# Kernel optimization log

Hardware: AMD Instinct MI355X
Metric: run time of the kernel (lower is better)

The kernel has to match this reference:

```python
import jax, jax.numpy as jnp
import numpy as np

B, TE, TD, H = 8, 512, 256, 256  # batch, enc len, dec len, hidden (He==Hd)

def setup_inputs() -> dict:
    key = jax.random.key(0)
    k1, k2, k3, k4, k5 = jax.random.split(key, 5)
    # Keras 'uniform' initializer: U(-0.05, 0.05)
    u = lambda k, s: jax.random.uniform(k, s, jnp.float32, -0.05, 0.05)
    return {
        "encoder_out_seq": jax.random.normal(k1, (B, TE, H), jnp.float32),
        "decoder_out_seq": jax.random.normal(k2, (B, TD, H), jnp.float32),
        "W_a": u(k3, (H, H)),
        "U_a": u(k4, (H, H)),
        "V_a": u(k5, (H, 1)),
    }

def reference(encoder_out_seq, decoder_out_seq, W_a, U_a, V_a):
    # Bahdanau additive attention, fully batched (same math as the per-step K.rnn loop)
    We = jnp.einsum('bih,hk->bik', encoder_out_seq, W_a)   # [B,Te,H]
    Uh = jnp.einsum('bjh,hk->bjk', decoder_out_seq, U_a)   # [B,Td,H]
    # energies: V_a^T tanh(We_i + Uh_j)  -> [B,Td,Te]
    t = jnp.tanh(We[:, None, :, :] + Uh[:, :, None, :])    # [B,Td,Te,H]
    e = jnp.einsum('bjih,h->bji', t, V_a[:, 0])             # [B,Td,Te]
    e = jax.nn.softmax(e, axis=-1)                          # softmax over encoder positions
    c = jnp.einsum('bji,bih->bjh', e, encoder_out_seq)      # [B,Td,H]
    return (c, e)
```

## Files before the change

kernel.cpp:

```cpp
#include <hip/hip_runtime.h>


#define BB 8
#define TE 512
#define TD 256
#define HH 256

#define EXP2F(x) __builtin_amdgcn_exp2f(x)
#define RCPF(x)  __builtin_amdgcn_rcpf(x)
#define KSCALE   2.8853900817779268f
#define NSC      (-2.8853900817779268f)

typedef __attribute__((ext_vector_type(8))) short short8_t;
typedef __attribute__((ext_vector_type(4))) float f32x4;

__device__ __forceinline__ unsigned short f2bf(float x) {
    unsigned int u = __float_as_uint(x);
    return (unsigned short)((u + 0x7FFFu + ((u >> 16) & 1u)) >> 16);
}
__device__ __forceinline__ float bf2f(unsigned short h) {
    return __uint_as_float(((unsigned int)h) << 16);
}

__global__ __launch_bounds__(256) void k_tw(
    const float* __restrict__ Wa, const float* __restrict__ Ua,
    unsigned short* __restrict__ Wth, unsigned short* __restrict__ Wtl)
{
    const int t    = threadIdx.x;
    const int s    = blockIdx.x >> 4;
    const int tile = blockIdx.x & 15;
    const int tk   = (tile >> 2) * 64;
    const int th   = (tile & 3) * 64;
    const float* W = s ? Ua : Wa;

    __shared__ float Ls[64][65];
    const int kr = t >> 4;
    const int hc = (t & 15) * 4;
    #pragma unroll
    for (int r = 0; r < 4; r++) {
        float4 v = *(const float4*)(W + (size_t)(tk + kr + 16 * r) * HH + th + hc);
        Ls[kr + 16 * r][hc + 0] = v.x; Ls[kr + 16 * r][hc + 1] = v.y;
        Ls[kr + 16 * r][hc + 2] = v.z; Ls[kr + 16 * r][hc + 3] = v.w;
    }
    __syncthreads();
    const int hr  = t >> 4;
    const int kc4 = (t & 15) * 4;
    #pragma unroll
    for (int r = 0; r < 4; r++) {
        const int hl = hr + 16 * r;
        float f0 = Ls[kc4 + 0][hl], f1 = Ls[kc4 + 1][hl];
        float f2 = Ls[kc4 + 2][hl], f3 = Ls[kc4 + 3][hl];
        ushort4 hi, lo;
        hi.x = f2bf(f0); lo.x = f2bf(f0 - bf2f(hi.x));
        hi.y = f2bf(f1); lo.y = f2bf(f1 - bf2f(hi.y));
        hi.z = f2bf(f2); lo.z = f2bf(f2 - bf2f(hi.z));
        hi.w = f2bf(f3); lo.w = f2bf(f3 - bf2f(hi.w));
        const size_t o = ((size_t)(s * 256 + th + hl)) * 256 + tk + kc4;
        *(ushort4*)(Wth + o) = hi;
        *(ushort4*)(Wtl + o) = lo;
    }
}

__global__ __launch_bounds__(256) void k_pre(
    const float* __restrict__ enc, const float* __restrict__ dec,
    const unsigned short* __restrict__ Wth, const unsigned short* __restrict__ Wtl,
    float* __restrict__ W4, float* __restrict__ Uhe)
{
    const int t  = threadIdx.x;
    const int it = blockIdx.x >> 2;
    const int ht = blockIdx.x & 3;
    const int i0 = it * 64;
    const int h0 = ht * 64;
    const bool is_enc = (i0 < BB * TE);
    const float* X = is_enc ? (enc + (size_t)i0 * HH)
                            : (dec + (size_t)(i0 - BB * TE) * HH);
    const int s = is_enc ? 0 : 1;
    const unsigned short* Ah = Wth + ((size_t)(s * 256 + h0)) * 256;
    const unsigned short* Al = Wtl + ((size_t)(s * 256 + h0)) * 256;

    __shared__ unsigned short At_h[64][40], At_l[64][40];
    __shared__ unsigned short Xs_h[64][40], Xs_l[64][40];

    const int sr = t >> 2;
    const int sq = (t & 3) * 8;

    const int wv = t >> 6, l = t & 63;
    const int wh = (wv & 1) * 32;
    const int wi = (wv >> 1) * 32;
    const int fr = l & 15;
    const int fk = (l >> 4) * 8;
    const int rq = l >> 4;

    f32x4 acc[2][2];
    #pragma unroll
    for (int a0 = 0; a0 < 2; a0++)
        #pragma unroll
        for (int a1 = 0; a1 < 2; a1++)
            acc[a0][a1] = (f32x4){0.f, 0.f, 0.f, 0.f};

    short8_t aH = *(const short8_t*)(Ah + (size_t)sr * 256 + sq);
    short8_t aL = *(const short8_t*)(Al + (size_t)sr * 256 + sq);
    float4   x0 = *(const float4*)(X + (size_t)sr * HH + sq);
    float4   x1 = *(const float4*)(X + (size_t)sr * HH + sq + 4);

    #pragma unroll
    for (int c = 0; c < 8; c++) {
        short8_t xh, xl;
        {
            unsigned short h;
            h = f2bf(x0.x); xh[0] = (short)h; xl[0] = (short)f2bf(x0.x - bf2f(h));
            h = f2bf(x0.y); xh[1] = (short)h; xl[1] = (short)f2bf(x0.y - bf2f(h));
            h = f2bf(x0.z); xh[2] = (short)h; xl[2] = (short)f2bf(x0.z - bf2f(h));
            h = f2bf(x0.w); xh[3] = (short)h; xl[3] = (short)f2bf(x0.w - bf2f(h));
            h = f2bf(x1.x); xh[4] = (short)h; xl[4] = (short)f2bf(x1.x - bf2f(h));
            h = f2bf(x1.y); xh[5] = (short)h; xl[5] = (short)f2bf(x1.y - bf2f(h));
            h = f2bf(x1.z); xh[6] = (short)h; xl[6] = (short)f2bf(x1.z - bf2f(h));
            h = f2bf(x1.w); xh[7] = (short)h; xl[7] = (short)f2bf(x1.w - bf2f(h));
        }
        __syncthreads();
        *(short8_t*)&At_h[sr][sq] = aH;
        *(short8_t*)&At_l[sr][sq] = aL;
        *(short8_t*)&Xs_h[sr][sq] = xh;
        *(short8_t*)&Xs_l[sr][sq] = xl;
        if (c < 7) {
            const int kc = (c + 1) * 32;
            aH = *(const short8_t*)(Ah + (size_t)sr * 256 + kc + sq);
            aL = *(const short8_t*)(Al + (size_t)sr * 256 + kc + sq);
            x0 = *(const float4*)(X + (size_t)sr * HH + kc + sq);
            x1 = *(const float4*)(X + (size_t)sr * HH + kc + sq + 4);
        }
        __syncthreads();
        #pragma unroll
        for (int fm = 0; fm < 2; fm++) {
            short8_t a_h = *(const short8_t*)&At_h[wh + 16 * fm + fr][fk];
            short8_t a_l = *(const short8_t*)&At_l[wh + 16 * fm + fr][fk];
            #pragma unroll
            for (int fn = 0; fn < 2; fn++) {
                short8_t b_h = *(const short8_t*)&Xs_h[wi + 16 * fn + fr][fk];
                short8_t b_l = *(const short8_t*)&Xs_l[wi + 16 * fn + fr][fk];
                acc[fm][fn] = __builtin_amdgcn_mfma_f32_16x16x32_bf16(a_h, b_h, acc[fm][fn], 0, 0, 0);
                acc[fm][fn] = __builtin_amdgcn_mfma_f32_16x16x32_bf16(a_h, b_l, acc[fm][fn], 0, 0, 0);
                acc[fm][fn] = __builtin_amdgcn_mfma_f32_16x16x32_bf16(a_l, b_h, acc[fm][fn], 0, 0, 0);
            }
        }
    }

    #pragma unroll
    for (int fm = 0; fm < 2; fm++) {
        #pragma unroll
        for (int fn = 0; fn < 2; fn++) {
            f32x4 v = acc[fm][fn];
            float4 o;
            o.x = EXP2F(v[0] * KSCALE);
            o.y = EXP2F(v[1] * KSCALE);
            o.z = EXP2F(v[2] * KSCALE);
            o.w = EXP2F(v[3] * KSCALE);
            const int ig = i0 + wi + 16 * fn + fr;
            const int hb = h0 + wh + 16 * fm + rq * 4;
            if (is_enc) {
                const int b  = ig >> 9;
                const int ib = ig & 511;
                const int hq = hb >> 2;
                *(float4*)(W4 + (((size_t)b * 64 + hq) * TE + ib) * 4) = o;
            } else {
                const int j = ig - BB * TE;
                *(float4*)(Uhe + (size_t)j * HH + hb) = o;
            }
        }
    }
}

__global__ __launch_bounds__(512) void k_attn(
    const float* __restrict__ enc, const float* __restrict__ W4,
    const float* __restrict__ Uhe, const float* __restrict__ Va,
    float* __restrict__ out_c, float* __restrict__ out_e)
{
    const int wv = threadIdx.x >> 6, lane = threadIdx.x & 63;
    const int b   = blockIdx.x & 7;
    const int j0  = (blockIdx.x >> 3) * 4;
    const int jj0 = b * TD + j0;

    __shared__ float sP[4][TE];
    __shared__ float sR[8][4][HH];

    const int i = (wv << 6) + lane;
    const float* wp = W4 + ((size_t)b * 64 * TE + i) * 4;
    const float* ua = Uhe + (size_t)jj0 * HH;
    const float* va = Va;

    float a0 = 0.f, a1 = 0.f, a2 = 0.f, a3 = 0.f;

#define QSTEP(ACC, U)                                                     \
    {                                                                     \
        float A_ = fmaf(w4.x, (U).x, 1.f);                                \
        float B_ = fmaf(w4.y, (U).y, 1.f);                                \
        float C_ = fmaf(w4.z, (U).z, 1.f);                                \
        float D_ = fmaf(w4.w, (U).w, 1.f);                                \
        float dAB = A_ * B_, dCD = C_ * D_;                               \
        float nAB = fmaf(v4.x, B_, v4.y * A_);                            \
        float nCD = fmaf(v4.z, D_, v4.w * C_);                            \
        float num = fmaf(nAB, dCD, nCD * dAB);                            \
        ACC = fmaf(num, RCPF(dAB * dCD), ACC);                            \
    }

#define ASTEP(Q, W4V)                                                     \
    {                                                                     \
        float4 w4 = W4V;                                                  \
        float4 v4 = *(const float4*)(va + 4 * (Q));                       \
        float4 u0 = *(const float4*)(ua + 4 * (Q));                       \
        float4 u1 = *(const float4*)(ua + HH + 4 * (Q));                  \
        float4 u2 = *(const float4*)(ua + 2 * HH + 4 * (Q));              \
        float4 u3 = *(const float4*)(ua + 3 * HH + 4 * (Q));              \
        QSTEP(a0, u0)                                                     \
        QSTEP(a1, u1)                                                     \
        QSTEP(a2, u2)                                                     \
        QSTEP(a3, u3)                                                     \
    }

    float4 wA = *(const float4*)(wp);
    float4 wB = *(const float4*)(wp + (size_t)TE * 4);
    for (int q = 0; q < 64; q += 2) {
        float4 wC = *(const float4*)(wp + (size_t)(q + 2) * TE * 4);
        float4 wD = *(const float4*)(wp + (size_t)(q + 3) * TE * 4);
        ASTEP(q, wA)
        ASTEP(q + 1, wB)
        wA = wC; wB = wD;
    }
#undef ASTEP
#undef QSTEP

    sP[0][i] = NSC * a0;
    sP[1][i] = NSC * a1;
    sP[2][i] = NSC * a2;
    sP[3][i] = NSC * a3;
    __syncthreads();

    if (wv < 4) {
        float ev[8];
        float m = -3.0e38f;
        #pragma unroll
        for (int k = 0; k < 8; k++) {
            ev[k] = sP[wv][lane + 64 * k];
            m = fmaxf(m, ev[k]);
        }
        #pragma unroll
        for (int off = 32; off; off >>= 1) m = fmaxf(m, __shfl_xor(m, off, 64));
        float s = 0.f;
        #pragma unroll
        for (int k = 0; k < 8; k++) { ev[k] = EXP2F(ev[k] - m); s += ev[k]; }
        #pragma unroll
        for (int off = 32; off; off >>= 1) s += __shfl_xor(s, off, 64);
        float rs = RCPF(s);
        float* oe = out_e + (size_t)(jj0 + wv) * TE;
        #pragma unroll
        for (int k = 0; k < 8; k++) {
            float p = ev[k] * rs;
            sP[wv][lane + 64 * k] = p;
            oe[lane + 64 * k] = p;
        }
    }
    __syncthreads();

    const int ib = wv << 6;
    const float* eb = enc + ((size_t)b * TE + ib) * HH + 4 * lane;
    float4 c0 = {0,0,0,0}, c1 = {0,0,0,0}, c2 = {0,0,0,0}, c3 = {0,0,0,0};

#define BSTEP(K, QV)                                                      \
    {                                                                     \
        float p0 = sP[0][ib + (K)];                                       \
        float p1 = sP[1][ib + (K)];                                       \
        float p2 = sP[2][ib + (K)];                                       \
        float p3 = sP[3][ib + (K)];                                       \
        float4 q = QV;                                                    \
        c0.x = fmaf(p0, q.x, c0.x); c0.y = fmaf(p0, q.y, c0.y);           \
        c0.z = fmaf(p0, q.z, c0.z); c0.w = fmaf(p0, q.w, c0.w);           \
        c1.x = fmaf(p1, q.x, c1.x); c1.y = fmaf(p1, q.y, c1.y);           \
        c1.z = fmaf(p1, q.z, c1.z); c1.w = fmaf(p1, q.w, c1.w);           \
        c2.x = fmaf(p2, q.x, c2.x); c2.y = fmaf(p2, q.y, c2.y);           \
        c2.z = fmaf(p2, q.z, c2.z); c2.w = fmaf(p2, q.w, c2.w);           \
        c3.x = fmaf(p3, q.x, c3.x); c3.y = fmaf(p3, q.y, c3.y);           \
        c3.z = fmaf(p3, q.z, c3.z); c3.w = fmaf(p3, q.w, c3.w);           \
    }

    float4 qA = *(const float4*)(eb);
    float4 qB = *(const float4*)(eb + (size_t)HH);
    for (int k = 0; k < 64; k += 2) {
        const int k2 = (k + 2 < 64) ? k + 2 : 62;
        const int k3 = (k + 3 < 64) ? k + 3 : 63;
        float4 qC = *(const float4*)(eb + (size_t)k2 * HH);
        float4 qD = *(const float4*)(eb + (size_t)k3 * HH);
        BSTEP(k, qA)
        BSTEP(k + 1, qB)
        qA = qC; qB = qD;
    }
#undef BSTEP

    *(float4*)&sR[wv][0][4 * lane] = c0;
    *(float4*)&sR[wv][1][4 * lane] = c1;
    *(float4*)&sR[wv][2][4 * lane] = c2;
    *(float4*)&sR[wv][3][4 * lane] = c3;
    __syncthreads();

    {
        const int jr = wv & 3;
        const int h2 = (wv >> 2) * 128 + 2 * lane;
        float sx = 0.f, sy = 0.f;
        #pragma unroll
        for (int ww = 0; ww < 8; ww++) {
            float2 tv = *(const float2*)&sR[ww][jr][h2];
            sx += tv.x; sy += tv.y;
        }
        float2 o; o.x = sx; o.y = sy;
        *(float2*)(out_c + (size_t)(jj0 + jr) * HH + h2) = o;
    }
}

extern "C" void kernel_launch(void* const* d_in, const int* in_sizes, int n_in,
                              void* d_out, int out_size, void* d_ws, size_t ws_size,
                              hipStream_t stream) {
    const float* enc = (const float*)d_in[0];
    const float* dec = (const float*)d_in[1];
    const float* Wa  = (const float*)d_in[2];
    const float* Ua  = (const float*)d_in[3];
    const float* Va  = (const float*)d_in[4];

    float* W4  = (float*)d_ws;
    float* Uhe = W4 + (size_t)BB * HH * TE;
    unsigned short* Wth = (unsigned short*)(Uhe + (size_t)BB * TD * HH);
    unsigned short* Wtl = Wth + 2 * 256 * 256;

    float* out_c = (float*)d_out;
    float* out_e = out_c + (size_t)BB * TD * HH;

    k_tw<<<32, 256, 0, stream>>>(Wa, Ua, Wth, Wtl);
    k_pre<<<384, 256, 0, stream>>>(enc, dec, Wth, Wtl, W4, Uhe);
    k_attn<<<BB * TD / 4, 512, 0, stream>>>(enc, W4, Uhe, Va, out_c, out_e);
}
```

Before: 107.4 us.

## Fuse weight transpose and bf16 split into projection GEMM kernel

Removes the separate weight-preprocessing kernel that transposed W_a/U_a and split them into bf16 hi/lo halves. The projection kernel now loads fp32 weight tiles directly, transposes them through a padded shared-memory buffer and converts them to hi/lo bf16 on the fly. This saves one kernel launch and a global round trip for the converted weights. In exchange, every block repeats the transpose and conversion work and each k-step gains an extra barrier.

```diff
diff --git a/kernel.cpp b/kernel.cpp
--- a/kernel.cpp
+++ b/kernel.cpp
@@ -22,48 +22,9 @@
     return __uint_as_float(((unsigned int)h) << 16);
 }
 
-__global__ __launch_bounds__(256) void k_tw(
-    const float* __restrict__ Wa, const float* __restrict__ Ua,
-    unsigned short* __restrict__ Wth, unsigned short* __restrict__ Wtl)
-{
-    const int t    = threadIdx.x;
-    const int s    = blockIdx.x >> 4;
-    const int tile = blockIdx.x & 15;
-    const int tk   = (tile >> 2) * 64;
-    const int th   = (tile & 3) * 64;
-    const float* W = s ? Ua : Wa;
-
-    __shared__ float Ls[64][65];
-    const int kr = t >> 4;
-    const int hc = (t & 15) * 4;
-    #pragma unroll
-    for (int r = 0; r < 4; r++) {
-        float4 v = *(const float4*)(W + (size_t)(tk + kr + 16 * r) * HH + th + hc);
-        Ls[kr + 16 * r][hc + 0] = v.x; Ls[kr + 16 * r][hc + 1] = v.y;
-        Ls[kr + 16 * r][hc + 2] = v.z; Ls[kr + 16 * r][hc + 3] = v.w;
-    }
-    __syncthreads();
-    const int hr  = t >> 4;
-    const int kc4 = (t & 15) * 4;
-    #pragma unroll
-    for (int r = 0; r < 4; r++) {
-        const int hl = hr + 16 * r;
-        float f0 = Ls[kc4 + 0][hl], f1 = Ls[kc4 + 1][hl];
-        float f2 = Ls[kc4 + 2][hl], f3 = Ls[kc4 + 3][hl];
-        ushort4 hi, lo;
-        hi.x = f2bf(f0); lo.x = f2bf(f0 - bf2f(hi.x));
-        hi.y = f2bf(f1); lo.y = f2bf(f1 - bf2f(hi.y));
-        hi.z = f2bf(f2); lo.z = f2bf(f2 - bf2f(hi.z));
-        hi.w = f2bf(f3); lo.w = f2bf(f3 - bf2f(hi.w));
-        const size_t o = ((size_t)(s * 256 + th + hl)) * 256 + tk + kc4;
-        *(ushort4*)(Wth + o) = hi;
-        *(ushort4*)(Wtl + o) = lo;
-    }
-}
-
 __global__ __launch_bounds__(256) void k_pre(
     const float* __restrict__ enc, const float* __restrict__ dec,
-    const unsigned short* __restrict__ Wth, const unsigned short* __restrict__ Wtl,
+    const float* __restrict__ Wa,  const float* __restrict__ Ua,
     float* __restrict__ W4, float* __restrict__ Uhe)
 {
     const int t  = threadIdx.x;
@@ -72,17 +33,18 @@
     const int i0 = it * 64;
     const int h0 = ht * 64;
     const bool is_enc = (i0 < BB * TE);
-    const float* X = is_enc ? (enc + (size_t)i0 * HH)
-                            : (dec + (size_t)(i0 - BB * TE) * HH);
-    const int s = is_enc ? 0 : 1;
-    const unsigned short* Ah = Wth + ((size_t)(s * 256 + h0)) * 256;
-    const unsigned short* Al = Wtl + ((size_t)(s * 256 + h0)) * 256;
+    const float* X  = is_enc ? (enc + (size_t)i0 * HH)
+                             : (dec + (size_t)(i0 - BB * TE) * HH);
+    const float* Wg = is_enc ? Wa : Ua;
 
     __shared__ unsigned short At_h[64][40], At_l[64][40];
     __shared__ unsigned short Xs_h[64][40], Xs_l[64][40];
+    __shared__ float T[32][66];
 
     const int sr = t >> 2;
     const int sq = (t & 3) * 8;
+    const int kr = t >> 3;
+    const int hc = (t & 7) * 8;
 
     const int wv = t >> 6, l = t & 63;
     const int wh = (wv & 1) * 32;
@@ -98,10 +60,10 @@
         for (int a1 = 0; a1 < 2; a1++)
             acc[a0][a1] = (f32x4){0.f, 0.f, 0.f, 0.f};
 
-    short8_t aH = *(const short8_t*)(Ah + (size_t)sr * 256 + sq);
-    short8_t aL = *(const short8_t*)(Al + (size_t)sr * 256 + sq);
-    float4   x0 = *(const float4*)(X + (size_t)sr * HH + sq);
-    float4   x1 = *(const float4*)(X + (size_t)sr * HH + sq + 4);
+    float4 x0  = *(const float4*)(X + (size_t)sr * HH + sq);
+    float4 x1  = *(const float4*)(X + (size_t)sr * HH + sq + 4);
+    float4 wf0 = *(const float4*)(Wg + (size_t)kr * HH + h0 + hc);
+    float4 wf1 = *(const float4*)(Wg + (size_t)kr * HH + h0 + hc + 4);
 
     #pragma unroll
     for (int c = 0; c < 8; c++) {
@@ -118,16 +80,36 @@
             h = f2bf(x1.w); xh[7] = (short)h; xl[7] = (short)f2bf(x1.w - bf2f(h));
         }
         __syncthreads();
-        *(short8_t*)&At_h[sr][sq] = aH;
-        *(short8_t*)&At_l[sr][sq] = aL;
         *(short8_t*)&Xs_h[sr][sq] = xh;
         *(short8_t*)&Xs_l[sr][sq] = xl;
+        {
+            float2 a, b;
+            a.x = wf0.x; a.y = wf0.y; b.x = wf0.z; b.y = wf0.w;
+            *(float2*)&T[kr][hc]     = a;
+            *(float2*)&T[kr][hc + 2] = b;
+            a.x = wf1.x; a.y = wf1.y; b.x = wf1.z; b.y = wf1.w;
+            *(float2*)&T[kr][hc + 4] = a;
+            *(float2*)&T[kr][hc + 6] = b;
+        }
+        __syncthreads();
+        {
+            short8_t ah_, al_;
+            #pragma unroll
+            for (int e = 0; e < 8; e++) {
+                float f = T[sq + e][sr];
+                unsigned short h = f2bf(f);
+                ah_[e] = (short)h;
+                al_[e] = (short)f2bf(f - bf2f(h));
+            }
+            *(short8_t*)&At_h[sr][sq] = ah_;
+            *(short8_t*)&At_l[sr][sq] = al_;
+        }
         if (c < 7) {
             const int kc = (c + 1) * 32;
-            aH = *(const short8_t*)(Ah + (size_t)sr * 256 + kc + sq);
-            aL = *(const short8_t*)(Al + (size_t)sr * 256 + kc + sq);
-            x0 = *(const float4*)(X + (size_t)sr * HH + kc + sq);
-            x1 = *(const float4*)(X + (size_t)sr * HH + kc + sq + 4);
+            x0  = *(const float4*)(X + (size_t)sr * HH + kc + sq);
+            x1  = *(const float4*)(X + (size_t)sr * HH + kc + sq + 4);
+            wf0 = *(const float4*)(Wg + (size_t)(kc + kr) * HH + h0 + hc);
+            wf1 = *(const float4*)(Wg + (size_t)(kc + kr) * HH + h0 + hc + 4);
         }
         __syncthreads();
         #pragma unroll
@@ -326,13 +308,10 @@
 
     float* W4  = (float*)d_ws;
     float* Uhe = W4 + (size_t)BB * HH * TE;
-    unsigned short* Wth = (unsigned short*)(Uhe + (size_t)BB * TD * HH);
-    unsigned short* Wtl = Wth + 2 * 256 * 256;
 
     float* out_c = (float*)d_out;
     float* out_e = out_c + (size_t)BB * TD * HH;
 
-    k_tw<<<32, 256, 0, stream>>>(Wa, Ua, Wth, Wtl);
-    k_pre<<<384, 256, 0, stream>>>(enc, dec, Wth, Wtl, W4, Uhe);
+    k_pre<<<384, 256, 0, stream>>>(enc, dec, Wa, Ua, W4, Uhe);
     k_attn<<<BB * TD / 4, 512, 0, stream>>>(enc, W4, Uhe, Va, out_c, out_e);
 }
```

Result: no change. 107.8 us (+0.4%).
